# Performance work log

Measured on AMD Instinct MI355X. Metric: run time of the kernel, lower is better.

## Reference

```python
import jax, jax.numpy as jnp
import numpy as np

B, N, DIN, DOUT = 16, 1024, 256, 256
NEG_SLOPE = 0.2


def setup_inputs() -> dict:
    key = jax.random.key(0)
    k1, k2, k3, k4 = jax.random.split(key, 4)
    h = jax.random.normal(k1, (B, N, DIN), dtype=jnp.float32)
    adj_mask = jax.random.randint(k2, (B, N, N), 0, 2, dtype=jnp.int32)
    # nn.Linear default init scale ~ 1/sqrt(fan_in)
    W = jax.random.normal(k3, (DOUT, DIN), dtype=jnp.float32) * (1.0 / np.sqrt(DIN))
    a = jax.random.normal(k4, (2 * DOUT,), dtype=jnp.float32) * (1.0 / np.sqrt(2 * DOUT))
    return {"h": h, "adj_mask": adj_mask, "W": W, "a": a}


def reference(h, adj_mask, W, a):
    # Wh: (B, N, DOUT)
    Wh = jnp.einsum("bnd,od->bno", h, W)
    # Decompose a([Wh_i || Wh_j]) = Wh_i @ a1 + Wh_j @ a2 (exact same math,
    # avoids materializing the (B,N,N,2*DOUT) concat tensor).
    d = Wh.shape[-1]
    a1, a2 = a[:d], a[d:]
    ei = Wh @ a1  # (B, N)
    ej = Wh @ a2  # (B, N)
    e = ei[:, :, None] + ej[:, None, :]  # (B, N, N)
    e = jnp.where(e > 0, e, NEG_SLOPE * e)  # leaky_relu(0.2)
    e = jnp.where(adj_mask == 0, -jnp.inf, e)
    alpha = jax.nn.softmax(e, axis=-1)
    # rows with no neighbors produce NaN -> zero them (matches masked_fill(isnan, 0))
    alpha = jnp.where(jnp.isnan(alpha), 0.0, alpha)
    # dropout omitted (eval mode / deterministic reference)
    h_out = jnp.einsum("bij,bjo->bio", alpha, Wh)
    return h_out
```

## Files before the change

kernel.cpp:

```cpp
#include <hip/hip_runtime.h>
#include <hip/hip_bf16.h>

constexpr int NB = 16;
constexpr int NN = 1024;
constexpr int DI = 256;
constexpr int DOv = 256;
constexpr float NEG = 0.2f;

#define GLOAD_LDS16(g, l) __builtin_amdgcn_global_load_lds( \
    (const __attribute__((address_space(1))) unsigned int*)(g), \
    (__attribute__((address_space(3))) unsigned int*)(l), 16, 0, 0)

__global__ __launch_bounds__(256, 2)
void gemm_wh(const float* __restrict__ h, const float* __restrict__ W,
             float* __restrict__ Wh) {
    __shared__ __align__(16) float Ask[32][132];
    __shared__ __align__(16) float Bs[32][68];
    const int t  = threadIdx.x;
    const int mb = blockIdx.x * 128;
    const int ob = blockIdx.y * 64;
    const int rg = t >> 4;
    const int cg = t & 15;
    const int m0 = rg * 8, o0 = cg * 4;
    float acc[8][4] = {};
    for (int k0 = 0; k0 < DI; k0 += 32) {
        __syncthreads();
        #pragma unroll
        for (int r = 0; r < 4; ++r) {
            int idx = r * 256 + t;
            int row = idx >> 3;
            int kk  = (idx & 7) * 4;
            float4 v = *(const float4*)&h[(size_t)(mb + row) * DI + k0 + kk];
            Ask[kk+0][row] = v.x; Ask[kk+1][row] = v.y;
            Ask[kk+2][row] = v.z; Ask[kk+3][row] = v.w;
        }
        #pragma unroll
        for (int r = 0; r < 2; ++r) {
            int idx = r * 256 + t;
            int row = idx >> 3;
            int kk  = (idx & 7) * 4;
            float4 u = *(const float4*)&W[(size_t)(ob + row) * DI + k0 + kk];
            Bs[kk+0][row] = u.x; Bs[kk+1][row] = u.y;
            Bs[kk+2][row] = u.z; Bs[kk+3][row] = u.w;
        }
        __syncthreads();
        #pragma unroll
        for (int k = 0; k < 32; ++k) {
            float4 a0 = *(const float4*)&Ask[k][m0];
            float4 a1 = *(const float4*)&Ask[k][m0 + 4];
            float4 bv = *(const float4*)&Bs[k][o0];
            float av[8] = {a0.x,a0.y,a0.z,a0.w,a1.x,a1.y,a1.z,a1.w};
            #pragma unroll
            for (int i = 0; i < 8; ++i) {
                acc[i][0] += av[i]*bv.x; acc[i][1] += av[i]*bv.y;
                acc[i][2] += av[i]*bv.z; acc[i][3] += av[i]*bv.w;
            }
        }
    }
    #pragma unroll
    for (int i = 0; i < 8; ++i) {
        float4 v = make_float4(acc[i][0], acc[i][1], acc[i][2], acc[i][3]);
        *(float4*)&Wh[(size_t)(mb + m0 + i) * DOv + ob + o0] = v;
    }
}

__global__ __launch_bounds__(256)
void ei_ej(const float* __restrict__ Wh, const float* __restrict__ a,
           float* __restrict__ ei, float* __restrict__ ej) {
    const int t = threadIdx.x;
    const int w = t >> 6, l = t & 63;
    const int row = blockIdx.x * 4 + w;
    float4 wv = *(const float4*)&Wh[(size_t)row * DOv + l * 4];
    float4 a1 = *(const float4*)&a[l * 4];
    float4 a2 = *(const float4*)&a[DOv + l * 4];
    float s1 = wv.x*a1.x + wv.y*a1.y + wv.z*a1.z + wv.w*a1.w;
    float s2 = wv.x*a2.x + wv.y*a2.y + wv.z*a2.z + wv.w*a2.w;
    #pragma unroll
    for (int off = 32; off; off >>= 1) {
        s1 += __shfl_xor(s1, off);
        s2 += __shfl_xor(s2, off);
    }
    if (l == 0) { ei[row] = s1; ej[row] = s2; }
}

constexpr int RI = 32;
constexpr int TJ = 32;
__global__ __launch_bounds__(512, 4)
void gat_attn(const float* __restrict__ Wh, const float* __restrict__ ei,
              const float* __restrict__ ej, const int* __restrict__ adj,
              float* __restrict__ out) {
    __shared__ __align__(16) float whs[TJ * DOv];
    __shared__ __align__(16) float ps[RI][TJ + 4];
    __shared__ float eis[RI];
    __shared__ float ejs[NN];
    __shared__ float ls[RI];

    const int t = threadIdx.x;
    const int swz = (blockIdx.x & 7) * 64 + (blockIdx.x >> 3);
    const int b  = swz >> 5;
    const int ib = (swz & 31) * RI;

    *(float2*)&ejs[t * 2] = *(const float2*)&ej[(size_t)b * NN + t * 2];
    if (t < RI) eis[t] = ei[(size_t)b * NN + ib + t];

    const int erow = t >> 4;
    const int ej0  = (t & 15) * 2;
    const int rg = t >> 6;
    const int cg = t & 63;
    const int m0 = rg * 4;
    const int o0 = cg * 4;

    float acc[4][4] = {};
    float lsum = 0.f;

    const float* whsrc = Wh + (size_t)b * NN * DOv;
    const int*   arow  = adj + ((size_t)b * NN + ib + erow) * NN;
    const float  eiv   = ei[(size_t)b * NN + ib + erow];

    for (int jt = 0; jt < NN; jt += TJ) {
        __syncthreads();
        const float* src = whsrc + (size_t)jt * DOv;
        #pragma unroll
        for (int r = 0; r < 4; ++r) {
            int idx = r * 512 + t;
            GLOAD_LDS16(src + idx * 4, whs + idx * 4);
        }
        int2   am  = *(const int2*)&arow[jt + ej0];
        float2 ejv = *(const float2*)&ejs[jt + ej0];
        float e0 = eiv + ejv.x; e0 = e0 > 0.f ? e0 : NEG * e0;
        float e1 = eiv + ejv.y; e1 = e1 > 0.f ? e1 : NEG * e1;
        float p0 = am.x ? __expf(e0) : 0.f;
        float p1 = am.y ? __expf(e1) : 0.f;
        *(float2*)&ps[erow][ej0] = make_float2(p0, p1);
        lsum += p0 + p1;
        __syncthreads();
        #pragma unroll
        for (int j2 = 0; j2 < TJ; j2 += 4) {
            float4 p4[4];
            #pragma unroll
            for (int k = 0; k < 4; ++k) p4[k] = *(const float4*)&ps[m0 + k][j2];
            const float* pf = (const float*)p4;
            #pragma unroll
            for (int u = 0; u < 4; ++u) {
                float4 w4 = *(const float4*)&whs[(j2 + u) * DOv + o0];
                #pragma unroll
                for (int k = 0; k < 4; ++k) {
                    float pv = pf[k * 4 + u];
                    acc[k][0] += pv * w4.x; acc[k][1] += pv * w4.y;
                    acc[k][2] += pv * w4.z; acc[k][3] += pv * w4.w;
                }
            }
        }
    }

    #pragma unroll
    for (int off = 8; off; off >>= 1) lsum += __shfl_xor(lsum, off);
    if ((t & 15) == 0) ls[erow] = lsum;
    __syncthreads();

    #pragma unroll
    for (int k = 0; k < 4; ++k) {
        float lv = ls[m0 + k];
        float iv = lv > 0.f ? 1.0f / lv : 0.f;
        float4 v = make_float4(acc[k][0]*iv, acc[k][1]*iv, acc[k][2]*iv, acc[k][3]*iv);
        *(float4*)&out[((size_t)b * NN + ib + m0 + k) * DOv + o0] = v;
    }
}

extern "C" void kernel_launch(void* const* d_in, const int* in_sizes, int n_in,
                              void* d_out, int out_size, void* d_ws, size_t ws_size,
                              hipStream_t stream) {
    const float* h   = (const float*)d_in[0];
    const int*   adj = (const int*)d_in[1];
    const float* W   = (const float*)d_in[2];
    const float* a   = (const float*)d_in[3];
    float* out = (float*)d_out;

    float* Wh = (float*)d_ws;
    float* ei = Wh + (size_t)NB * NN * DOv;
    float* ej = ei + (size_t)NB * NN;

    gemm_wh<<<dim3((NB * NN) / 128, DOv / 64), 256, 0, stream>>>(h, W, Wh);
    ei_ej<<<(NB * NN) / 4, 256, 0, stream>>>(Wh, a, ei, ej);
    gat_attn<<<NB * NN / RI, 512, 0, stream>>>(Wh, ei, ej, adj, out);
}
```

Baseline: 256.5 us.

## Double-buffer Wh tiles in attention kernel and prefetch GEMM operands into registers

The attention kernel now keeps two LDS buffers for the Wh tile and the probability tile. The async global-to-LDS load for tile i+2 and the exp/mask work for tile i+1 overlap with the FMA work on tile i, so there is only one barrier per tile instead of two. The Wh GEMM also stages its next K-slice in registers while it computes on the current LDS slice. The cost is roughly double the LDS use in the attention kernel, which lowers how many blocks can stay resident per CU, plus extra registers in the GEMM.

```diff
diff --git a/kernel.cpp b/kernel.cpp
--- a/kernel.cpp
+++ b/kernel.cpp
@@ -23,27 +23,44 @@
     const int cg = t & 15;
     const int m0 = rg * 8, o0 = cg * 4;
     float acc[8][4] = {};
-    for (int k0 = 0; k0 < DI; k0 += 32) {
+    float4 ra[4], rb[2];
+
+    auto loadAB = [&](int k0) {
+        #pragma unroll
+        for (int r = 0; r < 4; ++r) {
+            int idx = r * 256 + t;
+            int row = idx >> 3, kk = (idx & 7) * 4;
+            ra[r] = *(const float4*)&h[(size_t)(mb + row) * DI + k0 + kk];
+        }
+        #pragma unroll
+        for (int r = 0; r < 2; ++r) {
+            int idx = r * 256 + t;
+            int row = idx >> 3, kk = (idx & 7) * 4;
+            rb[r] = *(const float4*)&W[(size_t)(ob + row) * DI + k0 + kk];
+        }
+    };
+    auto writeAB = [&]() {
+        #pragma unroll
+        for (int r = 0; r < 4; ++r) {
+            int idx = r * 256 + t;
+            int row = idx >> 3, kk = (idx & 7) * 4;
+            Ask[kk+0][row] = ra[r].x; Ask[kk+1][row] = ra[r].y;
+            Ask[kk+2][row] = ra[r].z; Ask[kk+3][row] = ra[r].w;
+        }
+        #pragma unroll
+        for (int r = 0; r < 2; ++r) {
+            int idx = r * 256 + t;
+            int row = idx >> 3, kk = (idx & 7) * 4;
+            Bs[kk+0][row] = rb[r].x; Bs[kk+1][row] = rb[r].y;
+            Bs[kk+2][row] = rb[r].z; Bs[kk+3][row] = rb[r].w;
+        }
+    };
+
+    loadAB(0);
+    writeAB();
+    for (int kb = 0; kb < 8; ++kb) {
         __syncthreads();
-        #pragma unroll
-        for (int r = 0; r < 4; ++r) {
-            int idx = r * 256 + t;
-            int row = idx >> 3;
-            int kk  = (idx & 7) * 4;
-            float4 v = *(const float4*)&h[(size_t)(mb + row) * DI + k0 + kk];
-            Ask[kk+0][row] = v.x; Ask[kk+1][row] = v.y;
-            Ask[kk+2][row] = v.z; Ask[kk+3][row] = v.w;
-        }
-        #pragma unroll
-        for (int r = 0; r < 2; ++r) {
-            int idx = r * 256 + t;
-            int row = idx >> 3;
-            int kk  = (idx & 7) * 4;
-            float4 u = *(const float4*)&W[(size_t)(ob + row) * DI + k0 + kk];
-            Bs[kk+0][row] = u.x; Bs[kk+1][row] = u.y;
-            Bs[kk+2][row] = u.z; Bs[kk+3][row] = u.w;
-        }
-        __syncthreads();
+        if (kb < 7) loadAB((kb + 1) * 32);
         #pragma unroll
         for (int k = 0; k < 32; ++k) {
             float4 a0 = *(const float4*)&Ask[k][m0];
@@ -56,6 +73,8 @@
                 acc[i][2] += av[i]*bv.z; acc[i][3] += av[i]*bv.w;
             }
         }
+        __syncthreads();
+        if (kb < 7) writeAB();
     }
     #pragma unroll
     for (int i = 0; i < 8; ++i) {
@@ -89,9 +108,8 @@
 void gat_attn(const float* __restrict__ Wh, const float* __restrict__ ei,
               const float* __restrict__ ej, const int* __restrict__ adj,
               float* __restrict__ out) {
-    __shared__ __align__(16) float whs[TJ * DOv];
-    __shared__ __align__(16) float ps[RI][TJ + 4];
-    __shared__ float eis[RI];
+    __shared__ __align__(16) float whs[2][TJ * DOv];
+    __shared__ __align__(16) float ps[2][RI][TJ + 4];
     __shared__ float ejs[NN];
     __shared__ float ls[RI];
 
@@ -101,14 +119,12 @@
     const int ib = (swz & 31) * RI;
 
     *(float2*)&ejs[t * 2] = *(const float2*)&ej[(size_t)b * NN + t * 2];
-    if (t < RI) eis[t] = ei[(size_t)b * NN + ib + t];
 
     const int erow = t >> 4;
     const int ej0  = (t & 15) * 2;
     const int rg = t >> 6;
-    const int cg = t & 63;
     const int m0 = rg * 4;
-    const int o0 = cg * 4;
+    const int o0 = (t & 63) * 4;
 
     float acc[4][4] = {};
     float lsum = 0.f;
@@ -116,41 +132,63 @@
     const float* whsrc = Wh + (size_t)b * NN * DOv;
     const int*   arow  = adj + ((size_t)b * NN + ib + erow) * NN;
     const float  eiv   = ei[(size_t)b * NN + ib + erow];
-
-    for (int jt = 0; jt < NN; jt += TJ) {
-        __syncthreads();
-        const float* src = whsrc + (size_t)jt * DOv;
+    int2 am;
+
+    auto STAGE = [&](int buf, int tile) {
+        const float* src = whsrc + (size_t)tile * TJ * DOv;
+        float* dst = whs[buf];
         #pragma unroll
         for (int r = 0; r < 4; ++r) {
             int idx = r * 512 + t;
-            GLOAD_LDS16(src + idx * 4, whs + idx * 4);
-        }
-        int2   am  = *(const int2*)&arow[jt + ej0];
-        float2 ejv = *(const float2*)&ejs[jt + ej0];
+            GLOAD_LDS16(src + idx * 4, dst + idx * 4);
+        }
+    };
+    auto EPHASE = [&](int tile, int buf) {
+        float2 ejv = *(const float2*)&ejs[tile * TJ + ej0];
         float e0 = eiv + ejv.x; e0 = e0 > 0.f ? e0 : NEG * e0;
         float e1 = eiv + ejv.y; e1 = e1 > 0.f ? e1 : NEG * e1;
         float p0 = am.x ? __expf(e0) : 0.f;
         float p1 = am.y ? __expf(e1) : 0.f;
-        *(float2*)&ps[erow][ej0] = make_float2(p0, p1);
+        *(float2*)&ps[buf][erow][ej0] = make_float2(p0, p1);
         lsum += p0 + p1;
-        __syncthreads();
-        #pragma unroll
-        for (int j2 = 0; j2 < TJ; j2 += 4) {
-            float4 p4[4];
+    };
+
+    STAGE(0, 0);
+    am = *(const int2*)&arow[ej0];
+    __syncthreads();
+    STAGE(1, 1);
+    EPHASE(0, 0);
+    am = *(const int2*)&arow[TJ + ej0];
+    __syncthreads();
+
+    for (int i = 0; i < 32; ++i) {
+        const int cur = i & 1;
+        if (i + 1 < 32) {
+            EPHASE(i + 1, cur ^ 1);
+            if (i + 2 < 32) am = *(const int2*)&arow[(i + 2) * TJ + ej0];
+        }
+        {
+            const float* whc = whs[cur];
             #pragma unroll
-            for (int k = 0; k < 4; ++k) p4[k] = *(const float4*)&ps[m0 + k][j2];
-            const float* pf = (const float*)p4;
-            #pragma unroll
-            for (int u = 0; u < 4; ++u) {
-                float4 w4 = *(const float4*)&whs[(j2 + u) * DOv + o0];
+            for (int j2 = 0; j2 < TJ; j2 += 4) {
+                float4 p4[4];
                 #pragma unroll
-                for (int k = 0; k < 4; ++k) {
-                    float pv = pf[k * 4 + u];
-                    acc[k][0] += pv * w4.x; acc[k][1] += pv * w4.y;
-                    acc[k][2] += pv * w4.z; acc[k][3] += pv * w4.w;
+                for (int k = 0; k < 4; ++k) p4[k] = *(const float4*)&ps[cur][m0 + k][j2];
+                const float* pf = (const float*)p4;
+                #pragma unroll
+                for (int u = 0; u < 4; ++u) {
+                    float4 w4 = *(const float4*)&whc[(j2 + u) * DOv + o0];
+                    #pragma unroll
+                    for (int k = 0; k < 4; ++k) {
+                        float pv = pf[k * 4 + u];
+                        acc[k][0] += pv * w4.x; acc[k][1] += pv * w4.y;
+                        acc[k][2] += pv * w4.z; acc[k][3] += pv * w4.w;
+                    }
                 }
             }
         }
+        __syncthreads();
+        if (i + 2 < 32) STAGE(cur, i + 2);
     }
 
     #pragma unroll
```

After: 650.3 us. 154% more time.

## Double-buffer GEMM via direct LDS loads and stream Wh from global in attention

Applied to the files above, without the earlier changes.

The Wh GEMM moves to 512 threads with a 4x4 micro-tile. It loads h and W straight into XOR-swizzled LDS using global_load_lds and double-buffers the K stages, so the next tile's loads overlap the current FMAs and one barrier per stage is dropped. The attention kernel no longer stages Wh tiles in LDS and reads them directly from global (served by cache). It double-buffers the probability tile and prefetches the adjacency two tiles ahead. This trades LDS traffic and barriers for more global and cache load pressure in the inner loop.

```diff
diff --git a/kernel.cpp b/kernel.cpp
--- a/kernel.cpp
+++ b/kernel.cpp
@@ -11,57 +11,69 @@
     (const __attribute__((address_space(1))) unsigned int*)(g), \
     (__attribute__((address_space(3))) unsigned int*)(l), 16, 0, 0)
 
-__global__ __launch_bounds__(256, 2)
+__global__ __launch_bounds__(512, 4)
 void gemm_wh(const float* __restrict__ h, const float* __restrict__ W,
              float* __restrict__ Wh) {
-    __shared__ __align__(16) float Ask[32][132];
-    __shared__ __align__(16) float Bs[32][68];
+    __shared__ __align__(16) float4 Asl[2][1024];
+    __shared__ __align__(16) float4 Bsl[2][512];
     const int t  = threadIdx.x;
     const int mb = blockIdx.x * 128;
     const int ob = blockIdx.y * 64;
     const int rg = t >> 4;
     const int cg = t & 15;
-    const int m0 = rg * 8, o0 = cg * 4;
-    float acc[8][4] = {};
-    for (int k0 = 0; k0 < DI; k0 += 32) {
-        __syncthreads();
-        #pragma unroll
-        for (int r = 0; r < 4; ++r) {
-            int idx = r * 256 + t;
-            int row = idx >> 3;
-            int kk  = (idx & 7) * 4;
-            float4 v = *(const float4*)&h[(size_t)(mb + row) * DI + k0 + kk];
-            Ask[kk+0][row] = v.x; Ask[kk+1][row] = v.y;
-            Ask[kk+2][row] = v.z; Ask[kk+3][row] = v.w;
-        }
+    const int m0 = rg * 4, o0 = cg * 4;
+    float acc[4][4] = {};
+
+    auto STAGE = [&](int buf, int k0) {
         #pragma unroll
         for (int r = 0; r < 2; ++r) {
-            int idx = r * 256 + t;
-            int row = idx >> 3;
-            int kk  = (idx & 7) * 4;
-            float4 u = *(const float4*)&W[(size_t)(ob + row) * DI + k0 + kk];
-            Bs[kk+0][row] = u.x; Bs[kk+1][row] = u.y;
-            Bs[kk+2][row] = u.z; Bs[kk+3][row] = u.w;
+            int s = r * 512 + t;
+            int m = s >> 3;
+            int kg = (s & 7) ^ ((s >> 6) & 7);
+            GLOAD_LDS16(&h[(size_t)(mb + m) * DI + k0 + kg * 4], (float*)&Asl[buf][s]);
+        }
+        {
+            int s = t;
+            int o = s >> 3;
+            int kg = (s & 7) ^ ((s >> 5) & 7);
+            GLOAD_LDS16(&W[(size_t)(ob + o) * DI + k0 + kg * 4], (float*)&Bsl[buf][s]);
+        }
+    };
+
+    STAGE(0, 0);
+    __syncthreads();
+    for (int kb = 0; kb < 8; ++kb) {
+        const int cur = kb & 1;
+        if (kb < 7) STAGE(cur ^ 1, (kb + 1) * 32);
+        #pragma unroll
+        for (int kg = 0; kg < 8; ++kg) {
+            float4 bf[4], af[4];
+            #pragma unroll
+            for (int c = 0; c < 4; ++c) {
+                int o = o0 + c;
+                bf[c] = Bsl[cur][o * 8 + (kg ^ ((o >> 2) & 7))];
+            }
+            #pragma unroll
+            for (int i = 0; i < 4; ++i) {
+                int m = m0 + i;
+                af[i] = Asl[cur][m * 8 + (kg ^ ((m >> 3) & 7))];
+            }
+            #pragma unroll
+            for (int i = 0; i < 4; ++i)
+                #pragma unroll
+                for (int c = 0; c < 4; ++c) {
+                    acc[i][c] += af[i].x * bf[c].x;
+                    acc[i][c] += af[i].y * bf[c].y;
+                    acc[i][c] += af[i].z * bf[c].z;
+                    acc[i][c] += af[i].w * bf[c].w;
+                }
         }
         __syncthreads();
-        #pragma unroll
-        for (int k = 0; k < 32; ++k) {
-            float4 a0 = *(const float4*)&Ask[k][m0];
-            float4 a1 = *(const float4*)&Ask[k][m0 + 4];
-            float4 bv = *(const float4*)&Bs[k][o0];
-            float av[8] = {a0.x,a0.y,a0.z,a0.w,a1.x,a1.y,a1.z,a1.w};
-            #pragma unroll
-            for (int i = 0; i < 8; ++i) {
-                acc[i][0] += av[i]*bv.x; acc[i][1] += av[i]*bv.y;
-                acc[i][2] += av[i]*bv.z; acc[i][3] += av[i]*bv.w;
-            }
-        }
     }
     #pragma unroll
-    for (int i = 0; i < 8; ++i) {
-        float4 v = make_float4(acc[i][0], acc[i][1], acc[i][2], acc[i][3]);
-        *(float4*)&Wh[(size_t)(mb + m0 + i) * DOv + ob + o0] = v;
-    }
+    for (int i = 0; i < 4; ++i)
+        *(float4*)&Wh[(size_t)(mb + m0 + i) * DOv + ob + o0] =
+            make_float4(acc[i][0], acc[i][1], acc[i][2], acc[i][3]);
 }
 
 __global__ __launch_bounds__(256)
@@ -89,9 +101,7 @@
 void gat_attn(const float* __restrict__ Wh, const float* __restrict__ ei,
               const float* __restrict__ ej, const int* __restrict__ adj,
               float* __restrict__ out) {
-    __shared__ __align__(16) float whs[TJ * DOv];
-    __shared__ __align__(16) float ps[RI][TJ + 4];
-    __shared__ float eis[RI];
+    __shared__ __align__(16) float ps[2][RI][TJ + 4];
     __shared__ float ejs[NN];
     __shared__ float ls[RI];
 
@@ -101,48 +111,49 @@
     const int ib = (swz & 31) * RI;
 
     *(float2*)&ejs[t * 2] = *(const float2*)&ej[(size_t)b * NN + t * 2];
-    if (t < RI) eis[t] = ei[(size_t)b * NN + ib + t];
 
     const int erow = t >> 4;
     const int ej0  = (t & 15) * 2;
     const int rg = t >> 6;
-    const int cg = t & 63;
     const int m0 = rg * 4;
-    const int o0 = cg * 4;
+    const int o0 = (t & 63) * 4;
 
     float acc[4][4] = {};
     float lsum = 0.f;
 
-    const float* whsrc = Wh + (size_t)b * NN * DOv;
+    const float* wbase = Wh + (size_t)b * NN * DOv + o0;
     const int*   arow  = adj + ((size_t)b * NN + ib + erow) * NN;
     const float  eiv   = ei[(size_t)b * NN + ib + erow];
 
-    for (int jt = 0; jt < NN; jt += TJ) {
-        __syncthreads();
-        const float* src = whsrc + (size_t)jt * DOv;
-        #pragma unroll
-        for (int r = 0; r < 4; ++r) {
-            int idx = r * 512 + t;
-            GLOAD_LDS16(src + idx * 4, whs + idx * 4);
-        }
-        int2   am  = *(const int2*)&arow[jt + ej0];
-        float2 ejv = *(const float2*)&ejs[jt + ej0];
+    auto EPHASE = [&](int tile, int buf, int2 am) {
+        float2 ejv = *(const float2*)&ejs[tile * TJ + ej0];
         float e0 = eiv + ejv.x; e0 = e0 > 0.f ? e0 : NEG * e0;
         float e1 = eiv + ejv.y; e1 = e1 > 0.f ? e1 : NEG * e1;
         float p0 = am.x ? __expf(e0) : 0.f;
         float p1 = am.y ? __expf(e1) : 0.f;
-        *(float2*)&ps[erow][ej0] = make_float2(p0, p1);
+        *(float2*)&ps[buf][erow][ej0] = make_float2(p0, p1);
         lsum += p0 + p1;
-        __syncthreads();
+    };
+
+    int2 am0 = *(const int2*)&arow[ej0];
+    int2 amc = *(const int2*)&arow[TJ + ej0];
+    __syncthreads();
+    EPHASE(0, 0, am0);
+    __syncthreads();
+
+    for (int i = 0; i < 32; ++i) {
+        const int cur = i & 1;
+        if (i + 1 < 32) EPHASE(i + 1, cur ^ 1, amc);
+        if (i + 2 < 32) amc = *(const int2*)&arow[(i + 2) * TJ + ej0];
         #pragma unroll
         for (int j2 = 0; j2 < TJ; j2 += 4) {
             float4 p4[4];
             #pragma unroll
-            for (int k = 0; k < 4; ++k) p4[k] = *(const float4*)&ps[m0 + k][j2];
+            for (int k = 0; k < 4; ++k) p4[k] = *(const float4*)&ps[cur][m0 + k][j2];
             const float* pf = (const float*)p4;
             #pragma unroll
             for (int u = 0; u < 4; ++u) {
-                float4 w4 = *(const float4*)&whs[(j2 + u) * DOv + o0];
+                float4 w4 = *(const float4*)&wbase[(size_t)(i * TJ + j2 + u) * DOv];
                 #pragma unroll
                 for (int k = 0; k < 4; ++k) {
                     float pv = pf[k * 4 + u];
@@ -151,6 +162,7 @@
                 }
             }
         }
+        __syncthreads();
     }
 
     #pragma unroll
@@ -162,8 +174,8 @@
     for (int k = 0; k < 4; ++k) {
         float lv = ls[m0 + k];
         float iv = lv > 0.f ? 1.0f / lv : 0.f;
-        float4 v = make_float4(acc[k][0]*iv, acc[k][1]*iv, acc[k][2]*iv, acc[k][3]*iv);
-        *(float4*)&out[((size_t)b * NN + ib + m0 + k) * DOv + o0] = v;
+        *(float4*)&out[((size_t)b * NN + ib + m0 + k) * DOv + o0] =
+            make_float4(acc[k][0]*iv, acc[k][1]*iv, acc[k][2]*iv, acc[k][3]*iv);
     }
 }
 
@@ -180,7 +192,7 @@
     float* ei = Wh + (size_t)NB * NN * DOv;
     float* ej = ei + (size_t)NB * NN;
 
-    gemm_wh<<<dim3((NB * NN) / 128, DOv / 64), 256, 0, stream>>>(h, W, Wh);
+    gemm_wh<<<dim3((NB * NN) / 128, DOv / 64), 512, 0, stream>>>(h, W, Wh);
     ei_ej<<<(NB * NN) / 4, 256, 0, stream>>>(Wh, a, ei, ej);
     gat_attn<<<NB * NN / RI, 512, 0, stream>>>(Wh, ei, ej, adj, out);
 }
```

New measurement: 489.7 us. 90.9% more time.
